# Kernel optimization log

Measured on AMD Instinct MI355X. Metric: run time of the kernel, lower is better.

The kernel has to match this reference:

```python
import jax, jax.numpy as jnp
import numpy as np

L = 6          # topological levels
NPL = 50000    # nodes per level
K = 8          # in-degree of each non-root node
FEAT = 32
H = 128


def setup_inputs() -> dict:
    key = jax.random.key(0)
    ks = jax.random.split(key, 12)
    rng = np.random.default_rng(0)
    # layered DAG: level l nodes are ids [l*NPL, (l+1)*NPL); each non-root node
    # has K parents sampled from the previous level. Edge blocks are contiguous
    # and sorted by dst (matches topological processing order).
    src_l, dst_l = [], []
    for l in range(1, L):
        dst_l.append(np.repeat(np.arange(l * NPL, (l + 1) * NPL, dtype=np.int64), K))
        src_l.append(rng.integers((l - 1) * NPL, l * NPL, size=NPL * K, dtype=np.int64))
    src = jnp.asarray(np.concatenate(src_l))
    dst = jnp.asarray(np.concatenate(dst_l))

    def lin(k, fin, fout):
        return jax.random.normal(k, (fin, fout), jnp.float32) / np.float32(np.sqrt(fin))

    inp = {
        "node_feats": jax.random.normal(ks[0], (L * NPL, FEAT), jnp.float32),
        "src": src,
        "dst": dst,
        "W_embed": lin(ks[1], FEAT, H), "b_embed": jnp.zeros((H,), jnp.float32),
        "W_mp0": lin(ks[2], H, H), "b_mp0": jnp.zeros((H,), jnp.float32),
        "W_mp1": lin(ks[3], H, H), "b_mp1": jnp.zeros((H,), jnp.float32),
        "W_mp_cat": jax.vmap(lambda k: lin(k, 2 * H, H))(jax.random.split(ks[4], 4)),
        "b_mp_cat": jnp.zeros((4, H), jnp.float32),
        "W_ne0": lin(ks[5], 2 * H, H), "b_ne0": jnp.zeros((H,), jnp.float32),
        "W_ne1": lin(ks[6], H, H), "b_ne1": jnp.zeros((H,), jnp.float32),
        "W_ne_cat": jax.vmap(lambda k: lin(k, 2 * H, H))(jax.random.split(ks[7], 4)),
        "b_ne_cat": jnp.zeros((4, H), jnp.float32),
    }
    return inp


def reference(node_feats, src, dst, W_embed, b_embed, W_mp0, b_mp0, W_mp1, b_mp1,
              W_mp_cat, b_mp_cat, W_ne0, b_ne0, W_ne1, b_ne1, W_ne_cat, b_ne_cat):
    # apply_func's embed step (tanh(embed_op(feats))) for every node
    base = jnp.tanh(node_feats @ W_embed + b_embed)          # [N, H]
    embeds = [base[:NPL]]                                    # level 0: no mailbox
    for l in range(1, L):
        e0, e1 = (l - 1) * NPL * K, l * NPL * K              # this level's edge block
        s = src[e0:e1] - (l - 1) * NPL                       # local src ids in level l-1
        d = dst[e0:e1] - l * NPL                             # local dst ids in level l
        # mailbox sum: sum of predecessor embeds per dst node
        msgs = jax.ops.segment_sum(embeds[l - 1][s], d, num_segments=NPL)  # [NPL, H]
        # redux_func: 6 stacked tanh linears with concat skip to r0
        r0 = jnp.tanh(msgs @ W_mp0 + b_mp0)
        r = jnp.tanh(r0 @ W_mp1 + b_mp1)
        for i in range(4):
            r = jnp.tanh(jnp.concatenate([r, r0], -1) @ W_mp_cat[i] + b_mp_cat[i])
        # apply_func: combine embed with reduced messages via 6 stacked tanh linears
        blk = base[l * NPL:(l + 1) * NPL]
        c0 = jnp.tanh(jnp.concatenate([blk, r], -1) @ W_ne0 + b_ne0)
        e = jnp.tanh(c0 @ W_ne1 + b_ne1)
        for i in range(4):
            e = jnp.tanh(jnp.concatenate([e, c0], -1) @ W_ne_cat[i] + b_ne_cat[i])
        embeds.append(e)
    return jnp.concatenate(embeds, axis=0)                   # [N, H] bwd_node_embeds
```

## Files before the change

kernel.cpp:

```cpp
#include <hip/hip_runtime.h>

#define NPL 50000
#define KE 8
#define FEAT 32
#define H 128

typedef unsigned short u16;
typedef __attribute__((ext_vector_type(8))) short bf16x8;
typedef __attribute__((ext_vector_type(8))) unsigned short us8;
typedef __attribute__((ext_vector_type(16))) float f32x16;

__device__ __forceinline__ float bf2f(u16 u) {
    union { unsigned int i; float f; } v; v.i = ((unsigned int)u) << 16; return v.f;
}
__device__ __forceinline__ float fast_tanh(float x) {
    float e2 = __expf(2.0f * x);
    return 1.0f - 2.0f / (e2 + 1.0f);
}
__device__ __forceinline__ void f32_split_bf16(float x, u16& hi, u16& lo) {
    union { float f; unsigned u; } v; v.f = x;
    hi = (u16)(v.u >> 16);
    union { float f; unsigned u; } h; h.u = v.u & 0xFFFF0000u;
    union { float f; unsigned u; } r; r.f = x - h.f;
    lo = (u16)(r.u >> 16);
}

__device__ __forceinline__ bool weights_are_f32(const void* wv) {
    const u16* w = (const u16*)wv;
    int c = 0;
    #pragma unroll
    for (int i = 0; i < 64; ++i) c += (((w[2 * i] >> 7) & 0xFF) >= 131) ? 1 : 0;
    return c >= 4;
}
__device__ __forceinline__ bool src_is_i64(const int* s) {
    const int TOT = NPL * KE * 5;
    int zc = 0;
    #pragma unroll
    for (int i = 0; i < 32; ++i) zc += (s[TOT - 64 + 2 * i + 1] == 0) ? 1 : 0;
    return zc >= 16;
}
__device__ __forceinline__ float bias_at(const void* b, int off, bool f32) {
    return f32 ? ((const float*)b)[off] : bf2f(((const u16*)b)[off]);
}

__global__ __launch_bounds__(256) void embed_kernel(
    const void* __restrict__ nf, unsigned nf_row0,
    const void* __restrict__ Wg, const void* __restrict__ bg,
    float* __restrict__ outf)
{
    const bool f32in = weights_are_f32(Wg);
    __shared__ float sW[FEAT * H];
    __shared__ float snf[8][FEAT];
    const int tid = threadIdx.x;
    const int row0 = blockIdx.x * 8;

    if (f32in) {
        const float* Wf = (const float*)Wg;
        #pragma unroll
        for (int t = 0; t < 16; ++t) { int i = tid + t * 256; sW[i] = Wf[i]; }
    } else {
        const u16* Wh = (const u16*)Wg;
        #pragma unroll
        for (int t = 0; t < 16; ++t) { int i = tid + t * 256; sW[i] = bf2f(Wh[i]); }
    }
    {
        int r = tid >> 5, j = tid & 31;
        size_t gi = (size_t)(nf_row0 + row0 + r) * FEAT + j;
        snf[r][j] = f32in ? ((const float*)nf)[gi] : bf2f(((const u16*)nf)[gi]);
    }
    __syncthreads();

    const int c = tid & 127, rg = tid >> 7;
    const float bias = f32in ? ((const float*)bg)[c] : bf2f(((const u16*)bg)[c]);
    #pragma unroll
    for (int ir = 0; ir < 4; ++ir) {
        int r = ir * 2 + rg;
        float acc = bias;
        #pragma unroll
        for (int j = 0; j < FEAT; ++j) acc = fmaf(snf[r][j], sW[j * H + c], acc);
        outf[(size_t)(row0 + r) * H + c] = fast_tanh(acc);
    }
}

#define PW_MP0   0u
#define PW_MP1   (32u * 1024u)
#define PW_NE1   (64u * 1024u)
#define PW_NE0   (96u * 1024u)
#define PW_MPCAT (160u * 1024u)
#define PW_NECAT (416u * 1024u)
#define PW_EMB   (672u * 1024u)
#define PREW_BYTES ((size_t)680 * 2048)

__global__ __launch_bounds__(256) void preconv_kernel(
    const void* __restrict__ Wmp0, const void* __restrict__ Wmp1,
    const void* __restrict__ Wne1, const void* __restrict__ Wne0,
    const void* __restrict__ Wmpcat, const void* __restrict__ Wnecat,
    const void* __restrict__ Wembed,
    u16* __restrict__ preW)
{
    const bool f32w = weights_are_f32(Wmp0);
    const int fid = blockIdx.x * 4 + (threadIdx.x >> 6);
    const int lane = threadIdx.x & 63;
    const void* src; size_t eoff = 0; int nt, kk;
    if (fid >= 672) {
        int lf = fid - 672;
        src = Wembed; nt = lf >> 1; kk = lf & 1;
    } else if (fid < 96) {
        int m = fid >> 5, lf = fid & 31;
        src = (m == 0) ? Wmp0 : (m == 1) ? Wmp1 : Wne1;
        nt = lf >> 3; kk = lf & 7;
    } else {
        int g = fid - 96, m = g >> 6, lf = g & 63;
        if (m == 0)      { src = Wne0; }
        else if (m <= 4) { src = Wmpcat; eoff = (size_t)(m - 1) * 256 * H; }
        else             { src = Wnecat; eoff = (size_t)(m - 5) * 256 * H; }
        nt = lf >> 4; kk = lf & 15;
    }
    const int k0 = kk * 16 + ((lane >> 5) << 3);
    const int n  = nt * 32 + (lane & 31);
    us8 hv, lv;
    #pragma unroll
    for (int e = 0; e < 8; ++e) {
        size_t off = eoff + (size_t)(k0 + e) * H + n;
        float x = f32w ? ((const float*)src)[off] : bf2f(((const u16*)src)[off]);
        u16 h, l; f32_split_bf16(x, h, l);
        hv[e] = h; lv[e] = l;
    }
    u16* dst = preW + (size_t)fid * 1024 + lane * 8;
    *(us8*)dst         = hv;
    *(us8*)(dst + 512) = lv;
}

template <int KST>
__device__ __forceinline__ void mm_tiles(f32x16 acc[2],
    const u16* __restrict__ A1, const u16* __restrict__ A2,
    const u16* __restrict__ pW, int lane, int wc, bool wlo)
{
    const u16* fpb = pW + (unsigned)(wc * KST) * 1024u + (unsigned)(lane * 8);
    bf16x8 bh[4], bl[4];
    #pragma unroll
    for (int p = 0; p < 4; ++p) {
        bh[p] = *(const bf16x8*)(fpb + p * 1024u);
        if (wlo) bl[p] = *(const bf16x8*)(fpb + p * 1024u + 512u);
    }
    #pragma unroll
    for (int ks = 0; ks < KST; ++ks) {
        const int slot = ks & 3;
        bf16x8 cbh = bh[slot];
        bf16x8 cbl = bl[slot];
        if (ks + 4 < KST) {
            bh[slot] = *(const bf16x8*)(fpb + (ks + 4) * 1024u);
            if (wlo) bl[slot] = *(const bf16x8*)(fpb + (ks + 4) * 1024u + 512u);
        }
        const u16* A = (KST == 16 && ks >= 8) ? A2 : A1;
        const int kb = ((ks & 7) << 4) + ((lane >> 5) << 3);
        bf16x8 ah[2], al[2];
        #pragma unroll
        for (int i = 0; i < 2; ++i) {
            int r = i * 32 + (lane & 31);
            int off = (r << 7) + ((((kb >> 3) ^ (r & 15))) << 3);
            ah[i] = *(const bf16x8*)(A + off);
            al[i] = *(const bf16x8*)(A + 8192 + off);
        }
        acc[0] = __builtin_amdgcn_mfma_f32_32x32x16_bf16(ah[0], cbh, acc[0], 0, 0, 0);
        acc[1] = __builtin_amdgcn_mfma_f32_32x32x16_bf16(ah[1], cbh, acc[1], 0, 0, 0);
        acc[0] = __builtin_amdgcn_mfma_f32_32x32x16_bf16(al[0], cbh, acc[0], 0, 0, 0);
        acc[1] = __builtin_amdgcn_mfma_f32_32x32x16_bf16(al[1], cbh, acc[1], 0, 0, 0);
        if (wlo) {
            acc[0] = __builtin_amdgcn_mfma_f32_32x32x16_bf16(ah[0], cbl, acc[0], 0, 0, 0);
            acc[1] = __builtin_amdgcn_mfma_f32_32x32x16_bf16(ah[1], cbl, acc[1], 0, 0, 0);
        }
    }
}

__device__ __forceinline__ void mm_embed(f32x16 acc[2],
    const void* __restrict__ nf, unsigned nf_row0, int rb,
    const u16* __restrict__ pWe, int lane, int wc, bool nff, bool wlo)
{
    #pragma unroll
    for (int ks = 0; ks < 2; ++ks) {
        const int kb = (ks << 4) + ((lane >> 5) << 3);
        const u16* fp = pWe + (unsigned)(wc * 2 + ks) * 1024u + lane * 8;
        bf16x8 bh = *(const bf16x8*)fp;
        bf16x8 ah[2], al[2];
        #pragma unroll
        for (int i = 0; i < 2; ++i) {
            int gr = rb + i * 32 + (lane & 31);
            if (gr >= NPL) gr = 0;
            const size_t base = (size_t)(nf_row0 + gr) * FEAT + kb;
            float x[8];
            if (nff) {
                float4 v0 = *(const float4*)((const float*)nf + base);
                float4 v1 = *(const float4*)((const float*)nf + base + 4);
                x[0]=v0.x; x[1]=v0.y; x[2]=v0.z; x[3]=v0.w;
                x[4]=v1.x; x[5]=v1.y; x[6]=v1.z; x[7]=v1.w;
            } else {
                us8 u = *(const us8*)((const u16*)nf + base);
                #pragma unroll
                for (int e = 0; e < 8; ++e) x[e] = bf2f(u[e]);
            }
            #pragma unroll
            for (int e = 0; e < 8; ++e) {
                u16 h, l; f32_split_bf16(x[e], h, l);
                ah[i][e] = (short)h; al[i][e] = (short)l;
            }
        }
        #pragma unroll
        for (int i = 0; i < 2; ++i) {
            acc[i] = __builtin_amdgcn_mfma_f32_32x32x16_bf16(ah[i], bh, acc[i], 0, 0, 0);
            acc[i] = __builtin_amdgcn_mfma_f32_32x32x16_bf16(al[i], bh, acc[i], 0, 0, 0);
        }
        if (wlo) {
            bf16x8 bl = *(const bf16x8*)(fp + 512);
            #pragma unroll
            for (int i = 0; i < 2; ++i)
                acc[i] = __builtin_amdgcn_mfma_f32_32x32x16_bf16(ah[i], bl, acc[i], 0, 0, 0);
        }
    }
}

__device__ __forceinline__ void zacc(f32x16 acc[2]) {
    #pragma unroll
    for (int i = 0; i < 2; ++i)
        #pragma unroll
        for (int q = 0; q < 16; ++q) acc[i][q] = 0.f;
}

template <bool PRE>
__device__ __forceinline__ void epi_tile(f32x16 acc[2], const void* bias, int b_off,
                                         bool wlo, u16* __restrict__ D, int lane, int wc)
{
    const int c = wc * 32 + (lane & 31);
    const float bj = bias_at(bias, b_off + c, wlo);
    if (PRE) __syncthreads();
    #pragma unroll
    for (int i = 0; i < 2; ++i)
        #pragma unroll
        for (int q = 0; q < 16; ++q) {
            int r = i * 32 + (q & 3) + ((q >> 2) << 3) + ((lane >> 5) << 2);
            float v = fast_tanh(acc[i][q] + bj);
            u16 h, l; f32_split_bf16(v, h, l);
            int off = (r << 7) + (((c >> 3) ^ (r & 15)) << 3) + (c & 7);
            D[off] = h; D[8192 + off] = l;
        }
    __syncthreads();
}

__device__ __forceinline__ void epi_global(f32x16 acc[2], const void* bias, int b_off,
                                           bool wlo, float* __restrict__ E, int rb,
                                           int lane, int wc)
{
    const int c = wc * 32 + (lane & 31);
    const float bj = bias_at(bias, b_off + c, wlo);
    #pragma unroll
    for (int i = 0; i < 2; ++i)
        #pragma unroll
        for (int q = 0; q < 16; ++q) {
            int r = rb + i * 32 + (q & 3) + ((q >> 2) << 3) + ((lane >> 5) << 2);
            if (r < NPL) E[(size_t)r * H + c] = fast_tanh(acc[i][q] + bj);
        }
}

__global__ __launch_bounds__(256, 2) void layer_kernel(
    const float* __restrict__ P,
    float* __restrict__ E,
    const void* __restrict__ nf, unsigned nf_row0,
    const int* __restrict__ src, unsigned e0, int sbase,
    const u16* __restrict__ preW,
    const void* __restrict__ Wdet,
    const void* __restrict__ b_embed,
    const void* __restrict__ b_mp0, const void* __restrict__ b_mp1,
    const void* __restrict__ b_mpcat,
    const void* __restrict__ b_ne0, const void* __restrict__ b_ne1,
    const void* __restrict__ b_necat)
{
    const bool wlo = weights_are_f32(Wdet);
    const bool nff = weights_are_f32(nf);
    const bool s64 = src_is_i64(src);

    __shared__ __align__(16) u16 T[32768];
    u16* S0 = T;
    u16* S1 = T + 16384;

    const int tid = threadIdx.x;
    const int lane = tid & 63;
    const int wc = tid >> 6;
    const int rb = blockIdx.x * 64;

    #pragma unroll
    for (int it = 0; it < 4; ++it) {
        int slot = it * 256 + tid;
        int dl = slot >> 4, co = slot & 15;
        int d = rb + dl; if (d >= NPL) d = NPL - 1;
        const unsigned eb = e0 + (unsigned)d * KE;
        int skv[KE];
        #pragma unroll
        for (int k = 0; k < KE; ++k)
            skv[k] = (s64 ? src[2u * (eb + k)] : src[eb + k]) - sbase;
        float4 v0[KE], v1[KE];
        #pragma unroll
        for (int k = 0; k < KE; ++k) {
            const float* pr = P + (size_t)skv[k] * H + co * 8;
            v0[k] = *(const float4*)pr;
            v1[k] = *(const float4*)(pr + 4);
        }
        float a[8];
        #pragma unroll
        for (int q = 0; q < 8; ++q) a[q] = 0.f;
        #pragma unroll
        for (int k = 0; k < KE; ++k) {
            a[0] += v0[k].x; a[1] += v0[k].y; a[2] += v0[k].z; a[3] += v0[k].w;
            a[4] += v1[k].x; a[5] += v1[k].y; a[6] += v1[k].z; a[7] += v1[k].w;
        }
        us8 hv, lv;
        #pragma unroll
        for (int q = 0; q < 8; ++q) { u16 h, l; f32_split_bf16(a[q], h, l); hv[q] = h; lv[q] = l; }
        int off = (dl << 7) + ((co ^ (dl & 15)) << 3);
        *(us8*)(S0 + off) = hv;
        *(us8*)(S0 + 8192 + off) = lv;
    }
    __syncthreads();

    f32x16 acc[2];

    zacc(acc); mm_tiles<8>(acc, S0, S0, preW + PW_MP0, lane, wc, wlo);
    epi_tile<false>(acc, b_mp0, 0, wlo, S1, lane, wc);
    zacc(acc); mm_tiles<8>(acc, S1, S1, preW + PW_MP1, lane, wc, wlo);
    epi_tile<false>(acc, b_mp1, 0, wlo, S0, lane, wc);
    #pragma unroll 1
    for (int i = 0; i < 4; ++i) {
        zacc(acc); mm_tiles<16>(acc, S0, S1, preW + PW_MPCAT + (unsigned)i * 65536u, lane, wc, wlo);
        epi_tile<true>(acc, b_mpcat, i * H, wlo, S0, lane, wc);
    }
    zacc(acc); mm_embed(acc, nf, nf_row0, rb, preW + PW_EMB, lane, wc, nff, wlo);
    epi_tile<false>(acc, b_embed, 0, wlo, S1, lane, wc);
    zacc(acc); mm_tiles<16>(acc, S1, S0, preW + PW_NE0, lane, wc, wlo);
    epi_tile<true>(acc, b_ne0, 0, wlo, S1, lane, wc);
    zacc(acc); mm_tiles<8>(acc, S1, S1, preW + PW_NE1, lane, wc, wlo);
    epi_tile<false>(acc, b_ne1, 0, wlo, S0, lane, wc);
    #pragma unroll 1
    for (int i = 0; i < 3; ++i) {
        zacc(acc); mm_tiles<16>(acc, S0, S1, preW + PW_NECAT + (unsigned)i * 65536u, lane, wc, wlo);
        epi_tile<true>(acc, b_necat, i * H, wlo, S0, lane, wc);
    }
    zacc(acc); mm_tiles<16>(acc, S0, S1, preW + PW_NECAT + 3u * 65536u, lane, wc, wlo);
    epi_global(acc, b_necat, 3 * H, wlo, E, rb, lane, wc);
}

__global__ __launch_bounds__(256) void gather_kernel(
    const float* __restrict__ P, const int* __restrict__ src, unsigned e0,
    int base, float* __restrict__ M)
{
    const bool wide = src_is_i64(src);
    int idx = blockIdx.x * 256 + threadIdx.x;
    int d = idx >> 5, c4 = idx & 31;
    float ax = 0.f, ay = 0.f, az = 0.f, aw = 0.f;
    #pragma unroll
    for (int k = 0; k < KE; ++k) {
        unsigned e = e0 + (unsigned)d * KE + (unsigned)k;
        int sk = (wide ? src[2u * e] : src[e]) - base;
        float4 v = *((const float4*)(P + (size_t)sk * H) + c4);
        ax += v.x; ay += v.y; az += v.z; aw += v.w;
    }
    *((float4*)M + idx) = make_float4(ax, ay, az, aw);
}

template <int KTOT>
__global__ __launch_bounds__(256) void gemm_tanh(
    const float* __restrict__ X1, const float* __restrict__ X2,
    const void* __restrict__ Wgv, unsigned w_off,
    const void* __restrict__ bgv, unsigned b_off,
    float* __restrict__ outf)
{
    const bool f32w = weights_are_f32(Wgv);
    constexpr int KC = 64;
    __shared__ float sX[64 * 68];
    __shared__ float sW[KC * H];
    const int tid = threadIdx.x;
    const int ty = tid >> 4;
    const int tx = tid & 15;
    const int rb = blockIdx.x * 64;

    float acc[4][8];
    #pragma unroll
    for (int i = 0; i < 4; ++i)
        #pragma unroll
        for (int q = 0; q < 8; ++q) acc[i][q] = 0.f;

    for (int kc = 0; kc < KTOT; kc += KC) {
        const float* X = (KTOT == 256 && kc >= 128) ? X2 : X1;
        const int kb = (KTOT == 256 && kc >= 128) ? (kc - 128) : kc;
        #pragma unroll
        for (int t = 0; t < 4; ++t) {
            int e = tid + t * 256;
            int r = e >> 4, c4 = e & 15;
            int gr = rb + r;
            float4 v = make_float4(0.f, 0.f, 0.f, 0.f);
            if (gr < NPL) v = *((const float4*)(X + (size_t)gr * H + kb) + c4);
            *(float4*)(sX + r * 68 + c4 * 4) = v;
        }
        if (f32w) {
            const float* Wf = (const float*)Wgv + w_off;
            #pragma unroll
            for (int t = 0; t < 8; ++t) {
                int e = tid + t * 256;
                int kk = e >> 5, c4 = e & 31;
                float4 f = *((const float4*)(Wf + (size_t)(kc + kk) * H) + c4);
                *(float4*)(sW + kk * H + c4 * 4) = f;
            }
        } else {
            const u16* Wh = (const u16*)Wgv + w_off;
            #pragma unroll
            for (int t = 0; t < 8; ++t) {
                int e = tid + t * 256;
                int kk = e >> 5, c4 = e & 31;
                ushort4 u = *((const ushort4*)(Wh + (size_t)(kc + kk) * H) + c4);
                float4 f = make_float4(bf2f(u.x), bf2f(u.y), bf2f(u.z), bf2f(u.w));
                *(float4*)(sW + kk * H + c4 * 4) = f;
            }
        }
        __syncthreads();

        #pragma unroll 8
        for (int k = 0; k < KC; ++k) {
            const float4 w0 = *(const float4*)(sW + k * H + tx * 4);
            const float4 w1 = *(const float4*)(sW + k * H + 64 + tx * 4);
            float xs[4];
            xs[0] = sX[(ty * 4 + 0) * 68 + k];
            xs[1] = sX[(ty * 4 + 1) * 68 + k];
            xs[2] = sX[(ty * 4 + 2) * 68 + k];
            xs[3] = sX[(ty * 4 + 3) * 68 + k];
            #pragma unroll
            for (int i = 0; i < 4; ++i) {
                acc[i][0] = fmaf(xs[i], w0.x, acc[i][0]);
                acc[i][1] = fmaf(xs[i], w0.y, acc[i][1]);
                acc[i][2] = fmaf(xs[i], w0.z, acc[i][2]);
                acc[i][3] = fmaf(xs[i], w0.w, acc[i][3]);
                acc[i][4] = fmaf(xs[i], w1.x, acc[i][4]);
                acc[i][5] = fmaf(xs[i], w1.y, acc[i][5]);
                acc[i][6] = fmaf(xs[i], w1.z, acc[i][6]);
                acc[i][7] = fmaf(xs[i], w1.w, acc[i][7]);
            }
        }
        __syncthreads();
    }

    float b0v[4], b1v[4];
    if (f32w) {
        const float* bf_ = (const float*)bgv + b_off;
        float4 t0 = *((const float4*)bf_ + tx);
        float4 t1 = *((const float4*)bf_ + 16 + tx);
        b0v[0]=t0.x; b0v[1]=t0.y; b0v[2]=t0.z; b0v[3]=t0.w;
        b1v[0]=t1.x; b1v[1]=t1.y; b1v[2]=t1.z; b1v[3]=t1.w;
    } else {
        const u16* bh = (const u16*)bgv + b_off;
        ushort4 u0 = *((const ushort4*)bh + tx);
        ushort4 u1 = *((const ushort4*)bh + 16 + tx);
        b0v[0]=bf2f(u0.x); b0v[1]=bf2f(u0.y); b0v[2]=bf2f(u0.z); b0v[3]=bf2f(u0.w);
        b1v[0]=bf2f(u1.x); b1v[1]=bf2f(u1.y); b1v[2]=bf2f(u1.z); b1v[3]=bf2f(u1.w);
    }

    #pragma unroll
    for (int i = 0; i < 4; ++i) {
        int grow = rb + ty * 4 + i;
        if (grow >= NPL) continue;
        float4 o0, o1;
        o0.x = fast_tanh(acc[i][0] + b0v[0]);
        o0.y = fast_tanh(acc[i][1] + b0v[1]);
        o0.z = fast_tanh(acc[i][2] + b0v[2]);
        o0.w = fast_tanh(acc[i][3] + b0v[3]);
        o1.x = fast_tanh(acc[i][4] + b1v[0]);
        o1.y = fast_tanh(acc[i][5] + b1v[1]);
        o1.z = fast_tanh(acc[i][6] + b1v[2]);
        o1.w = fast_tanh(acc[i][7] + b1v[3]);
        *((float4*)(outf + (size_t)grow * H) + tx)      = o0;
        *((float4*)(outf + (size_t)grow * H) + 16 + tx) = o1;
    }
}

extern "C" void kernel_launch(void* const* d_in, const int* in_sizes, int n_in,
                              void* d_out, int out_size, void* d_ws, size_t ws_size,
                              hipStream_t stream) {
    const void* nf      = d_in[0];
    const int*  src     = (const int*)d_in[1];
    const void* W_embed = d_in[3];
    const void* b_embed = d_in[4];
    const void* W_mp0   = d_in[5];
    const void* b_mp0   = d_in[6];
    const void* W_mp1   = d_in[7];
    const void* b_mp1   = d_in[8];
    const void* W_mp_cat= d_in[9];
    const void* b_mp_cat= d_in[10];
    const void* W_ne0   = d_in[11];
    const void* b_ne0   = d_in[12];
    const void* W_ne1   = d_in[13];
    const void* b_ne1   = d_in[14];
    const void* W_ne_cat= d_in[15];
    const void* b_ne_cat= d_in[16];
    float* out = (float*)d_out;

    const size_t BLK = (size_t)NPL * H;
    const bool use_mfma = (d_ws != nullptr) && (ws_size >= PREW_BYTES);

    if (use_mfma) {
        u16* pw = (u16*)d_ws;
        embed_kernel<<<NPL / 8, 256, 0, stream>>>(nf, 0u, W_embed, b_embed, out);
        preconv_kernel<<<170, 256, 0, stream>>>(W_mp0, W_mp1, W_ne1, W_ne0,
                                                W_mp_cat, W_ne_cat, W_embed, pw);
        const int LG = (NPL + 63) / 64;
        for (int l = 1; l < 6; ++l) {
            layer_kernel<<<LG, 256, 0, stream>>>(
                out + (size_t)(l - 1) * BLK, out + (size_t)l * BLK,
                nf, (unsigned)(l * NPL),
                src, (unsigned)((l - 1) * NPL * KE), (l - 1) * NPL,
                pw, W_mp0,
                b_embed, b_mp0, b_mp1, b_mp_cat, b_ne0, b_ne1, b_ne_cat);
        }
        return;
    }

    const int GEMM_GRID = (NPL + 63) / 64;
    const int EMB_GRID  = NPL / 8;
    const int GAT_GRID  = NPL * 32 / 256;

    embed_kernel<<<EMB_GRID, 256, 0, stream>>>(nf, 0u, W_embed, b_embed, out);
    for (int l = 1; l < 6; ++l) {
        const float* P = out + (size_t)(l - 1) * BLK;
        float* A = out + (size_t)((l < 5) ? (l + 1) : 0) * BLK;
        float* B = out + (size_t)l * BLK;

        gather_kernel<<<GAT_GRID, 256, 0, stream>>>(P, src, (unsigned)((l - 1) * NPL * KE), (l - 1) * NPL, A);
        gemm_tanh<128><<<GEMM_GRID, 256, 0, stream>>>(A, (const float*)nullptr, W_mp0, 0u, b_mp0, 0u, A);
        gemm_tanh<128><<<GEMM_GRID, 256, 0, stream>>>(A, (const float*)nullptr, W_mp1, 0u, b_mp1, 0u, B);
        for (int i = 0; i < 4; ++i)
            gemm_tanh<256><<<GEMM_GRID, 256, 0, stream>>>(B, A, W_mp_cat, (unsigned)(i * 256 * H),
                                                          b_mp_cat, (unsigned)(i * H), B);
        embed_kernel<<<EMB_GRID, 256, 0, stream>>>(nf, (unsigned)(l * NPL), W_embed, b_embed, A);
        gemm_tanh<256><<<GEMM_GRID, 256, 0, stream>>>(A, B, W_ne0, 0u, b_ne0, 0u, A);
        gemm_tanh<128><<<GEMM_GRID, 256, 0, stream>>>(A, (const float*)nullptr, W_ne1, 0u, b_ne1, 0u, B);
        for (int i = 0; i < 4; ++i)
            gemm_tanh<256><<<GEMM_GRID, 256, 0, stream>>>(B, A, W_ne_cat, (unsigned)(i * 256 * H),
                                                          b_ne_cat, (unsigned)(i * H), B);
    }
    embed_kernel<<<EMB_GRID, 256, 0, stream>>>(nf, 0u, W_embed, b_embed, out);
}
```

Baseline: 1.056 ms.

## Transpose MFMA operands for vector epilogue, prefetch next weights and biases, hoist embed

The MFMA operand order is swapped so each lane's accumulator holds four consecutive output columns of one row. Epilogues can then write ushort4 to LDS and float4 to global memory instead of scattered scalar stores. The first weight fragments of the next matmul and its bias vector are prefetched while the current epilogue runs. The embed matmul is moved to the kernel start so its global loads overlap the gather phase. This costs extra live registers (the acc_blk accumulators and the prefetch buffers), which risks spills or lower occupancy under the launch bounds of two blocks.

```diff
diff --git a/kernel.cpp b/kernel.cpp
--- a/kernel.cpp
+++ b/kernel.cpp
@@ -131,18 +131,42 @@
     *(us8*)(dst + 512) = lv;
 }
 
+struct Pro { bf16x8 bh[4]; bf16x8 bl[4]; };
+
+__device__ __forceinline__ Pro load_pro(const u16* pW, int kst, int lane, int wc, bool wlo) {
+    Pro p;
+    const u16* fpb = pW + (unsigned)(wc * kst) * 1024u + (unsigned)(lane * 8);
+    #pragma unroll
+    for (int q = 0; q < 4; ++q) {
+        p.bh[q] = *(const bf16x8*)(fpb + q * 1024u);
+        if (wlo) p.bl[q] = *(const bf16x8*)(fpb + q * 1024u + 512u);
+    }
+    return p;
+}
+
+__device__ __forceinline__ void load_bias4(const void* bgv, int b_off, bool f32,
+                                           int lane, int wc, float4 bv[4]) {
+    const int cb = b_off + wc * 32 + ((lane >> 5) << 2);
+    #pragma unroll
+    for (int g = 0; g < 4; ++g) {
+        int c = cb + 8 * g;
+        if (f32) bv[g] = *(const float4*)((const float*)bgv + c);
+        else {
+            ushort4 u = *(const ushort4*)((const u16*)bgv + c);
+            bv[g] = make_float4(bf2f(u.x), bf2f(u.y), bf2f(u.z), bf2f(u.w));
+        }
+    }
+}
+
 template <int KST>
 __device__ __forceinline__ void mm_tiles(f32x16 acc[2],
     const u16* __restrict__ A1, const u16* __restrict__ A2,
-    const u16* __restrict__ pW, int lane, int wc, bool wlo)
+    const u16* __restrict__ pW, Pro pro, int lane, int wc, bool wlo)
 {
     const u16* fpb = pW + (unsigned)(wc * KST) * 1024u + (unsigned)(lane * 8);
     bf16x8 bh[4], bl[4];
     #pragma unroll
-    for (int p = 0; p < 4; ++p) {
-        bh[p] = *(const bf16x8*)(fpb + p * 1024u);
-        if (wlo) bl[p] = *(const bf16x8*)(fpb + p * 1024u + 512u);
-    }
+    for (int p = 0; p < 4; ++p) { bh[p] = pro.bh[p]; bl[p] = pro.bl[p]; }
     #pragma unroll
     for (int ks = 0; ks < KST; ++ks) {
         const int slot = ks & 3;
@@ -154,21 +178,21 @@
         }
         const u16* A = (KST == 16 && ks >= 8) ? A2 : A1;
         const int kb = ((ks & 7) << 4) + ((lane >> 5) << 3);
-        bf16x8 ah[2], al[2];
+        bf16x8 xh[2], xl[2];
         #pragma unroll
         for (int i = 0; i < 2; ++i) {
             int r = i * 32 + (lane & 31);
             int off = (r << 7) + ((((kb >> 3) ^ (r & 15))) << 3);
-            ah[i] = *(const bf16x8*)(A + off);
-            al[i] = *(const bf16x8*)(A + 8192 + off);
-        }
-        acc[0] = __builtin_amdgcn_mfma_f32_32x32x16_bf16(ah[0], cbh, acc[0], 0, 0, 0);
-        acc[1] = __builtin_amdgcn_mfma_f32_32x32x16_bf16(ah[1], cbh, acc[1], 0, 0, 0);
-        acc[0] = __builtin_amdgcn_mfma_f32_32x32x16_bf16(al[0], cbh, acc[0], 0, 0, 0);
-        acc[1] = __builtin_amdgcn_mfma_f32_32x32x16_bf16(al[1], cbh, acc[1], 0, 0, 0);
+            xh[i] = *(const bf16x8*)(A + off);
+            xl[i] = *(const bf16x8*)(A + 8192 + off);
+        }
+        acc[0] = __builtin_amdgcn_mfma_f32_32x32x16_bf16(cbh, xh[0], acc[0], 0, 0, 0);
+        acc[1] = __builtin_amdgcn_mfma_f32_32x32x16_bf16(cbh, xh[1], acc[1], 0, 0, 0);
+        acc[0] = __builtin_amdgcn_mfma_f32_32x32x16_bf16(cbh, xl[0], acc[0], 0, 0, 0);
+        acc[1] = __builtin_amdgcn_mfma_f32_32x32x16_bf16(cbh, xl[1], acc[1], 0, 0, 0);
         if (wlo) {
-            acc[0] = __builtin_amdgcn_mfma_f32_32x32x16_bf16(ah[0], cbl, acc[0], 0, 0, 0);
-            acc[1] = __builtin_amdgcn_mfma_f32_32x32x16_bf16(ah[1], cbl, acc[1], 0, 0, 0);
+            acc[0] = __builtin_amdgcn_mfma_f32_32x32x16_bf16(cbl, xh[0], acc[0], 0, 0, 0);
+            acc[1] = __builtin_amdgcn_mfma_f32_32x32x16_bf16(cbl, xh[1], acc[1], 0, 0, 0);
         }
     }
 }
@@ -182,7 +206,7 @@
         const int kb = (ks << 4) + ((lane >> 5) << 3);
         const u16* fp = pWe + (unsigned)(wc * 2 + ks) * 1024u + lane * 8;
         bf16x8 bh = *(const bf16x8*)fp;
-        bf16x8 ah[2], al[2];
+        bf16x8 xh[2], xl[2];
         #pragma unroll
         for (int i = 0; i < 2; ++i) {
             int gr = rb + i * 32 + (lane & 31);
@@ -202,19 +226,19 @@
             #pragma unroll
             for (int e = 0; e < 8; ++e) {
                 u16 h, l; f32_split_bf16(x[e], h, l);
-                ah[i][e] = (short)h; al[i][e] = (short)l;
+                xh[i][e] = (short)h; xl[i][e] = (short)l;
             }
         }
         #pragma unroll
         for (int i = 0; i < 2; ++i) {
-            acc[i] = __builtin_amdgcn_mfma_f32_32x32x16_bf16(ah[i], bh, acc[i], 0, 0, 0);
-            acc[i] = __builtin_amdgcn_mfma_f32_32x32x16_bf16(al[i], bh, acc[i], 0, 0, 0);
+            acc[i] = __builtin_amdgcn_mfma_f32_32x32x16_bf16(bh, xh[i], acc[i], 0, 0, 0);
+            acc[i] = __builtin_amdgcn_mfma_f32_32x32x16_bf16(bh, xl[i], acc[i], 0, 0, 0);
         }
         if (wlo) {
             bf16x8 bl = *(const bf16x8*)(fp + 512);
             #pragma unroll
             for (int i = 0; i < 2; ++i)
-                acc[i] = __builtin_amdgcn_mfma_f32_32x32x16_bf16(ah[i], bl, acc[i], 0, 0, 0);
+                acc[i] = __builtin_amdgcn_mfma_f32_32x32x16_bf16(bl, xh[i], acc[i], 0, 0, 0);
         }
     }
 }
@@ -227,38 +251,52 @@
 }
 
 template <bool PRE>
-__device__ __forceinline__ void epi_tile(f32x16 acc[2], const void* bias, int b_off,
-                                         bool wlo, u16* __restrict__ D, int lane, int wc)
-{
-    const int c = wc * 32 + (lane & 31);
-    const float bj = bias_at(bias, b_off + c, wlo);
+__device__ __forceinline__ void epi_tile(f32x16 acc[2], const float4 bv[4],
+                                         u16* __restrict__ D, int lane, int wc)
+{
     if (PRE) __syncthreads();
-    #pragma unroll
-    for (int i = 0; i < 2; ++i)
-        #pragma unroll
-        for (int q = 0; q < 16; ++q) {
-            int r = i * 32 + (q & 3) + ((q >> 2) << 3) + ((lane >> 5) << 2);
-            float v = fast_tanh(acc[i][q] + bj);
-            u16 h, l; f32_split_bf16(v, h, l);
-            int off = (r << 7) + (((c >> 3) ^ (r & 15)) << 3) + (c & 7);
-            D[off] = h; D[8192 + off] = l;
-        }
+    const int kb0 = wc * 32 + ((lane >> 5) << 2);
+    #pragma unroll
+    for (int i = 0; i < 2; ++i) {
+        const int r = i * 32 + (lane & 31);
+        #pragma unroll
+        for (int g = 0; g < 4; ++g) {
+            float v0 = fast_tanh(acc[i][g * 4 + 0] + bv[g].x);
+            float v1 = fast_tanh(acc[i][g * 4 + 1] + bv[g].y);
+            float v2 = fast_tanh(acc[i][g * 4 + 2] + bv[g].z);
+            float v3 = fast_tanh(acc[i][g * 4 + 3] + bv[g].w);
+            u16 h0,l0,h1,l1,h2,l2,h3,l3;
+            f32_split_bf16(v0,h0,l0); f32_split_bf16(v1,h1,l1);
+            f32_split_bf16(v2,h2,l2); f32_split_bf16(v3,h3,l3);
+            int k = kb0 + 8 * g;
+            int off = (r << 7) + (((k >> 3) ^ (r & 15)) << 3) + (k & 7);
+            *(ushort4*)(D + off)        = make_ushort4(h0, h1, h2, h3);
+            *(ushort4*)(D + 8192 + off) = make_ushort4(l0, l1, l2, l3);
+        }
+    }
     __syncthreads();
 }
 
-__device__ __forceinline__ void epi_global(f32x16 acc[2], const void* bias, int b_off,
-                                           bool wlo, float* __restrict__ E, int rb,
+__device__ __forceinline__ void epi_global(f32x16 acc[2], const float4 bv[4],
+                                           float* __restrict__ E, int rb,
                                            int lane, int wc)
 {
-    const int c = wc * 32 + (lane & 31);
-    const float bj = bias_at(bias, b_off + c, wlo);
-    #pragma unroll
-    for (int i = 0; i < 2; ++i)
-        #pragma unroll
-        for (int q = 0; q < 16; ++q) {
-            int r = rb + i * 32 + (q & 3) + ((q >> 2) << 3) + ((lane >> 5) << 2);
-            if (r < NPL) E[(size_t)r * H + c] = fast_tanh(acc[i][q] + bj);
-        }
+    const int kb0 = wc * 32 + ((lane >> 5) << 2);
+    #pragma unroll
+    for (int i = 0; i < 2; ++i) {
+        const int r = rb + i * 32 + (lane & 31);
+        if (r < NPL) {
+            #pragma unroll
+            for (int g = 0; g < 4; ++g) {
+                float4 o;
+                o.x = fast_tanh(acc[i][g * 4 + 0] + bv[g].x);
+                o.y = fast_tanh(acc[i][g * 4 + 1] + bv[g].y);
+                o.z = fast_tanh(acc[i][g * 4 + 2] + bv[g].z);
+                o.w = fast_tanh(acc[i][g * 4 + 3] + bv[g].w);
+                *(float4*)(E + (size_t)r * H + kb0 + 8 * g) = o;
+            }
+        }
+    }
 }
 
 __global__ __launch_bounds__(256, 2) void layer_kernel(
@@ -287,6 +325,10 @@
     const int wc = tid >> 6;
     const int rb = blockIdx.x * 64;
 
+    f32x16 acc_blk[2];
+    zacc(acc_blk);
+    mm_embed(acc_blk, nf, nf_row0, rb, preW + PW_EMB, lane, wc, nff, wlo);
+
     #pragma unroll
     for (int it = 0; it < 4; ++it) {
         int slot = it * 256 + tid;
@@ -319,32 +361,49 @@
         *(us8*)(S0 + off) = hv;
         *(us8*)(S0 + 8192 + off) = lv;
     }
+
+    Pro pro = load_pro(preW + PW_MP0, 8, lane, wc, wlo);
+    float4 bv[4];
+    load_bias4(b_mp0, 0, wlo, lane, wc, bv);
     __syncthreads();
 
     f32x16 acc[2];
 
-    zacc(acc); mm_tiles<8>(acc, S0, S0, preW + PW_MP0, lane, wc, wlo);
-    epi_tile<false>(acc, b_mp0, 0, wlo, S1, lane, wc);
-    zacc(acc); mm_tiles<8>(acc, S1, S1, preW + PW_MP1, lane, wc, wlo);
-    epi_tile<false>(acc, b_mp1, 0, wlo, S0, lane, wc);
+    zacc(acc); mm_tiles<8>(acc, S0, S0, preW + PW_MP0, pro, lane, wc, wlo);
+    pro = load_pro(preW + PW_MP1, 8, lane, wc, wlo);
+    epi_tile<false>(acc, bv, S1, lane, wc);
+    load_bias4(b_mp1, 0, wlo, lane, wc, bv);
+    zacc(acc); mm_tiles<8>(acc, S1, S1, preW + PW_MP1, pro, lane, wc, wlo);
+    pro = load_pro(preW + PW_MPCAT, 16, lane, wc, wlo);
+    epi_tile<false>(acc, bv, S0, lane, wc);
     #pragma unroll 1
     for (int i = 0; i < 4; ++i) {
-        zacc(acc); mm_tiles<16>(acc, S0, S1, preW + PW_MPCAT + (unsigned)i * 65536u, lane, wc, wlo);
-        epi_tile<true>(acc, b_mpcat, i * H, wlo, S0, lane, wc);
-    }
-    zacc(acc); mm_embed(acc, nf, nf_row0, rb, preW + PW_EMB, lane, wc, nff, wlo);
-    epi_tile<false>(acc, b_embed, 0, wlo, S1, lane, wc);
-    zacc(acc); mm_tiles<16>(acc, S1, S0, preW + PW_NE0, lane, wc, wlo);
-    epi_tile<true>(acc, b_ne0, 0, wlo, S1, lane, wc);
-    zacc(acc); mm_tiles<8>(acc, S1, S1, preW + PW_NE1, lane, wc, wlo);
-    epi_tile<false>(acc, b_ne1, 0, wlo, S0, lane, wc);
+        load_bias4(b_mpcat, i * H, wlo, lane, wc, bv);
+        zacc(acc); mm_tiles<16>(acc, S0, S1, preW + PW_MPCAT + (unsigned)i * 65536u, pro, lane, wc, wlo);
+        unsigned nxt = (i < 3) ? (PW_MPCAT + (unsigned)(i + 1) * 65536u) : PW_NE0;
+        pro = load_pro(preW + nxt, 16, lane, wc, wlo);
+        epi_tile<true>(acc, bv, S0, lane, wc);
+    }
+    load_bias4(b_embed, 0, wlo, lane, wc, bv);
+    epi_tile<false>(acc_blk, bv, S1, lane, wc);
+    load_bias4(b_ne0, 0, wlo, lane, wc, bv);
+    zacc(acc); mm_tiles<16>(acc, S1, S0, preW + PW_NE0, pro, lane, wc, wlo);
+    pro = load_pro(preW + PW_NE1, 8, lane, wc, wlo);
+    epi_tile<true>(acc, bv, S1, lane, wc);
+    load_bias4(b_ne1, 0, wlo, lane, wc, bv);
+    zacc(acc); mm_tiles<8>(acc, S1, S1, preW + PW_NE1, pro, lane, wc, wlo);
+    pro = load_pro(preW + PW_NECAT, 16, lane, wc, wlo);
+    epi_tile<false>(acc, bv, S0, lane, wc);
     #pragma unroll 1
     for (int i = 0; i < 3; ++i) {
-        zacc(acc); mm_tiles<16>(acc, S0, S1, preW + PW_NECAT + (unsigned)i * 65536u, lane, wc, wlo);
-        epi_tile<true>(acc, b_necat, i * H, wlo, S0, lane, wc);
-    }
-    zacc(acc); mm_tiles<16>(acc, S0, S1, preW + PW_NECAT + 3u * 65536u, lane, wc, wlo);
-    epi_global(acc, b_necat, 3 * H, wlo, E, rb, lane, wc);
+        load_bias4(b_necat, i * H, wlo, lane, wc, bv);
+        zacc(acc); mm_tiles<16>(acc, S0, S1, preW + PW_NECAT + (unsigned)i * 65536u, pro, lane, wc, wlo);
+        pro = load_pro(preW + PW_NECAT + (unsigned)(i + 1) * 65536u, 16, lane, wc, wlo);
+        epi_tile<true>(acc, bv, S0, lane, wc);
+    }
+    load_bias4(b_necat, 3 * H, wlo, lane, wc, bv);
+    zacc(acc); mm_tiles<16>(acc, S0, S1, preW + PW_NECAT + 3u * 65536u, pro, lane, wc, wlo);
+    epi_global(acc, bv, E, rb, lane, wc);
 }
 
 __global__ __launch_bounds__(256) void gather_kernel(
```

New measurement: 1.052 ms. About the same (-0.4%).
